# Kernel optimization log

Measured on AMD Instinct MI355X. Metric: run time of the kernel, lower is better.

## Reference

```python
import jax, jax.numpy as jnp
import numpy as np

N_NODES = 50000
N_EDGES = 1600000
N_GRAPHS = 64


def setup_inputs() -> dict:
    key = jax.random.key(0)
    ks = jax.random.split(key, 16)
    p = lambda k, shape: (jax.random.normal(k, shape, dtype=jnp.float32) * 0.05)
    x = jax.random.normal(ks[0], (N_NODES, 128), dtype=jnp.float32)
    edge_index = jax.random.randint(ks[1], (2, N_EDGES), 0, N_NODES, dtype=jnp.int32)
    edge_attr = jax.random.uniform(ks[2], (N_EDGES,), dtype=jnp.float32)
    batch = jnp.sort(jax.random.randint(ks[3], (N_NODES,), 0, N_GRAPHS, dtype=jnp.int32))
    return {
        'x': x, 'edge_index': edge_index, 'edge_attr': edge_attr, 'batch': batch,
        'W1': p(ks[4], (128, 128)), 'b1': jnp.zeros((128,), jnp.float32),
        'W2': p(ks[5], (128, 64)), 'b2': jnp.zeros((64,), jnp.float32),
        'gW1': p(ks[6], (64, 32)), 'gb1': jnp.zeros((32,), jnp.float32),
        'gW2': p(ks[7], (32, 1)), 'gb2': jnp.zeros((1,), jnp.float32),
        'fcW1': p(ks[8], (64, 128)), 'fcb1': jnp.zeros((128,), jnp.float32),
        'fcW2': p(ks[9], (128, 2)), 'fcb2': jnp.zeros((2,), jnp.float32),
    }


def gcn_conv(x, src, dst, ew, W, b):
    # PyG GCNConv with edge weights: add self-loops (weight 1), symmetric norm.
    xw = x @ W  # [N, out]
    deg = jax.ops.segment_sum(ew, dst, num_segments=N_NODES) + 1.0  # self-loop
    dinv = jnp.where(deg > 0, jax.lax.rsqrt(deg), 0.0)
    coef = dinv[src] * ew * dinv[dst]  # [E]
    agg = jax.ops.segment_sum(coef[:, None] * xw[src], dst, num_segments=N_NODES)
    agg = agg + (dinv * dinv)[:, None] * xw  # self-loop contribution
    return agg + b


def global_attention(x, batch, gW1, gb1, gW2, gb2):
    # gate_nn: Linear(64,32)->ReLU->Linear(32,1), segment-softmax over graphs
    g = (jax.nn.relu(x @ gW1 + gb1) @ gW2 + gb2)[:, 0]  # [N]
    gmax = jax.ops.segment_max(g, batch, num_segments=N_GRAPHS)
    ex = jnp.exp(g - gmax[batch])
    den = jax.ops.segment_sum(ex, batch, num_segments=N_GRAPHS)
    alpha = ex / den[batch]
    return jax.ops.segment_sum(alpha[:, None] * x, batch, num_segments=N_GRAPHS)


def reference(x, edge_index, edge_attr, batch, W1, b1, W2, b2,
              gW1, gb1, gW2, gb2, fcW1, fcb1, fcW2, fcb2):
    src, dst = edge_index[0], edge_index[1]
    h = jax.nn.relu(gcn_conv(x, src, dst, edge_attr, W1, b1))
    x1 = jax.nn.relu(gcn_conv(h, src, dst, edge_attr, W2, b2))
    x2 = global_attention(x1, batch, gW1, gb1, gW2, gb2)  # [G, 64]
    # dropout is identity in eval mode
    h2 = jax.nn.relu(x2 @ fcW1 + fcb1)
    logits = h2 @ fcW2 + fcb2
    return jax.nn.log_softmax(logits, axis=1)
```

## Files before the change

kernel.cpp:

```cpp
#include <hip/hip_runtime.h>
#include <hip/hip_bf16.h>
#include <hip/hip_fp16.h>

#define N_NODES 50000
#define N_EDGES 1600000
#define N_GRAPHS 64
#define G1BLKS 1563

__device__ __forceinline__ float coef_of(unsigned p) {
    return __half2float(__ushort_as_half((unsigned short)(p & 0xFFFFu)));
}

__global__ void mega1(const float* __restrict__ X, const float* __restrict__ W,
                      __half* __restrict__ Yh, const int* __restrict__ dst,
                      const float* __restrict__ ew,
                      unsigned long long* __restrict__ packed,
                      unsigned short* __restrict__ pos16) {
    __shared__ float Xl[32][132];
    if (blockIdx.x >= G1BLKS) {
        int e = (blockIdx.x - G1BLKS) * 256 + threadIdx.x;
        if (e < N_EDGES) {
            int d = __builtin_nontemporal_load(&dst[e]);
            float w = __builtin_nontemporal_load(&ew[e]);
            unsigned fix = (unsigned)(w * 16777216.0f);
            unsigned long long old = atomicAdd(&packed[d], 0x100000000ull | (unsigned long long)fix);
            pos16[e] = (unsigned short)(old >> 32);
        }
        return;
    }
    const int rt = threadIdx.x >> 5;
    const int ct = threadIdx.x & 31;
    const int base = blockIdx.x * 32;
    for (int i = threadIdx.x; i < 32 * 32; i += 256) {
        int rr = i >> 5, cc = (i & 31) << 2;
        int gr = base + rr;
        float4 v = (gr < N_NODES) ? *(const float4*)&X[(size_t)gr * 128 + cc]
                                  : make_float4(0.f, 0.f, 0.f, 0.f);
        Xl[rr][cc] = v.x; Xl[rr][cc + 1] = v.y; Xl[rr][cc + 2] = v.z; Xl[rr][cc + 3] = v.w;
    }
    __syncthreads();
    float acc[4][4] = {};
    for (int k = 0; k < 128; k += 4) {
        float4 a0 = *(const float4*)&Xl[rt * 4 + 0][k];
        float4 a1 = *(const float4*)&Xl[rt * 4 + 1][k];
        float4 a2 = *(const float4*)&Xl[rt * 4 + 2][k];
        float4 a3 = *(const float4*)&Xl[rt * 4 + 3][k];
        float4 w0 = *(const float4*)&W[(size_t)(k + 0) * 128 + ct * 4];
        float4 w1 = *(const float4*)&W[(size_t)(k + 1) * 128 + ct * 4];
        float4 w2 = *(const float4*)&W[(size_t)(k + 2) * 128 + ct * 4];
        float4 w3 = *(const float4*)&W[(size_t)(k + 3) * 128 + ct * 4];
        #define STEP(av, wv)  \
            acc[0][0] += av##0 * wv.x; acc[0][1] += av##0 * wv.y; acc[0][2] += av##0 * wv.z; acc[0][3] += av##0 * wv.w; \
            acc[1][0] += av##1 * wv.x; acc[1][1] += av##1 * wv.y; acc[1][2] += av##1 * wv.z; acc[1][3] += av##1 * wv.w; \
            acc[2][0] += av##2 * wv.x; acc[2][1] += av##2 * wv.y; acc[2][2] += av##2 * wv.z; acc[2][3] += av##2 * wv.w; \
            acc[3][0] += av##3 * wv.x; acc[3][1] += av##3 * wv.y; acc[3][2] += av##3 * wv.z; acc[3][3] += av##3 * wv.w;
        { float ax0=a0.x, ax1=a1.x, ax2=a2.x, ax3=a3.x; STEP(ax, w0) }
        { float ay0=a0.y, ay1=a1.y, ay2=a2.y, ay3=a3.y; STEP(ay, w1) }
        { float az0=a0.z, az1=a1.z, az2=a2.z, az3=a3.z; STEP(az, w2) }
        { float aw0=a0.w, aw1=a1.w, aw2=a2.w, aw3=a3.w; STEP(aw, w3) }
        #undef STEP
    }
    const int pc = ct >> 3;
    const int cw = (ct & 7) * 4;
    for (int i = 0; i < 4; ++i) {
        int gr = base + rt * 4 + i;
        if (gr < N_NODES) {
            ushort4 u;
            u.x = __half_as_ushort(__float2half(acc[i][0]));
            u.y = __half_as_ushort(__float2half(acc[i][1]));
            u.z = __half_as_ushort(__float2half(acc[i][2]));
            u.w = __half_as_ushort(__float2half(acc[i][3]));
            *(ushort4*)&Yh[((size_t)pc * N_NODES + gr) * 32 + cw] = u;
        }
    }
}

__global__ void block_sums_dinv(const unsigned long long* __restrict__ packed,
                                int* __restrict__ bsum, float* __restrict__ dinv) {
    __shared__ int s[256];
    int idx = blockIdx.x * 256 + threadIdx.x;
    int c = 0;
    if (idx < N_NODES) {
        unsigned long long p = packed[idx];
        c = (int)(p >> 32);
        dinv[idx] = rsqrtf((float)(unsigned)(p & 0xFFFFFFFFu) * (1.0f / 16777216.0f) + 1.0f);
    }
    s[threadIdx.x] = c;
    __syncthreads();
    for (int o = 128; o; o >>= 1) {
        if (threadIdx.x < o) s[threadIdx.x] += s[threadIdx.x + o];
        __syncthreads();
    }
    if (threadIdx.x == 0) bsum[blockIdx.x] = s[0];
}

__global__ void scan_bsums(const int* __restrict__ bsum, int* __restrict__ boff,
                           int nb, int* __restrict__ row_start_last) {
    __shared__ int s[256];
    int v = (threadIdx.x < nb) ? bsum[threadIdx.x] : 0;
    s[threadIdx.x] = v;
    __syncthreads();
    for (int o = 1; o < 256; o <<= 1) {
        int t = 0;
        if (threadIdx.x >= o) t = s[threadIdx.x - o];
        __syncthreads();
        s[threadIdx.x] += t;
        __syncthreads();
    }
    if (threadIdx.x < nb) boff[threadIdx.x] = s[threadIdx.x] - v;
    if (threadIdx.x == 0) *row_start_last = N_EDGES;
}

__global__ void scan_counts(const unsigned long long* __restrict__ packed,
                            const int* __restrict__ boff, int* __restrict__ row_start) {
    __shared__ int s[256];
    int idx = blockIdx.x * 256 + threadIdx.x;
    int v = (idx < N_NODES) ? (int)(packed[idx] >> 32) : 0;
    s[threadIdx.x] = v;
    __syncthreads();
    for (int o = 1; o < 256; o <<= 1) {
        int t = 0;
        if (threadIdx.x >= o) t = s[threadIdx.x - o];
        __syncthreads();
        s[threadIdx.x] += t;
        __syncthreads();
    }
    if (idx < N_NODES) row_start[idx] = boff[blockIdx.x] + s[threadIdx.x] - v;
}

__global__ void fill_direct(const int* __restrict__ src, const int* __restrict__ dst,
                            const float* __restrict__ ew, const unsigned short* __restrict__ pos16,
                            const int* __restrict__ row_start, const float* __restrict__ dinv,
                            unsigned* __restrict__ csr) {
    int e = blockIdx.x * 256 + threadIdx.x;
    if (e < N_EDGES) {
        int d = __builtin_nontemporal_load(&dst[e]);
        int s = __builtin_nontemporal_load(&src[e]);
        float w = __builtin_nontemporal_load(&ew[e]);
        int p = (int)__builtin_nontemporal_load(&pos16[e]);
        float coef = dinv[s] * w * dinv[d];
        csr[row_start[d] + p] = ((unsigned)s << 16) | __half_as_ushort(__float2half(coef));
    }
}

template<int NP, bool HOUT>
__global__ void agg_csr_pair(const int* __restrict__ row_start, const unsigned* __restrict__ csr,
                             const __half* __restrict__ xwh, const float* __restrict__ dinv,
                             const float* __restrict__ b, void* __restrict__ outp) {
    constexpr int OUT = NP * 32;
    const int c  = blockIdx.x % NP;
    const int nb = blockIdx.x / NP;
    const int n  = nb * 4 + (threadIdx.x >> 6);
    const int kk = threadIdx.x & 15;
    const int q  = (threadIdx.x >> 4) & 3;
    if (n >= N_NODES) return;
    const __half* __restrict__ bp = xwh + ((size_t)c * N_NODES) * 32 + 2 * kk;
    const int beg = row_start[n], end = row_start[n + 1];
    float ax = 0.f, ay = 0.f;
    int i = beg + q;
    for (; i + 12 < end; i += 16) {
        unsigned p0 = csr[i],     p1 = csr[i + 4];
        unsigned p2 = csr[i + 8], p3 = csr[i + 12];
        float2 f0 = __half22float2(*(const __half2*)(bp + (size_t)(p0 >> 16) * 32));
        float2 f1 = __half22float2(*(const __half2*)(bp + (size_t)(p1 >> 16) * 32));
        float2 f2 = __half22float2(*(const __half2*)(bp + (size_t)(p2 >> 16) * 32));
        float2 f3 = __half22float2(*(const __half2*)(bp + (size_t)(p3 >> 16) * 32));
        float e0 = coef_of(p0), e1 = coef_of(p1), e2 = coef_of(p2), e3 = coef_of(p3);
        ax += e0 * f0.x + e1 * f1.x + e2 * f2.x + e3 * f3.x;
        ay += e0 * f0.y + e1 * f1.y + e2 * f2.y + e3 * f3.y;
    }
    for (; i < end; i += 4) {
        unsigned p = csr[i];
        float2 f = __half22float2(*(const __half2*)(bp + (size_t)(p >> 16) * 32));
        float e = coef_of(p);
        ax += e * f.x; ay += e * f.y;
    }
    ax += __shfl_xor(ax, 16);  ay += __shfl_xor(ay, 16);
    ax += __shfl_xor(ax, 32);  ay += __shfl_xor(ay, 32);
    if (q == 0) {
        float2 sf = __half22float2(*(const __half2*)(bp + (size_t)n * 32));
        float dv = dinv[n];
        float dv2 = dv * dv;
        int kg = c * 32 + 2 * kk;
        float ox = fmaxf(ax + dv2 * sf.x + b[kg], 0.f);
        float oy = fmaxf(ay + dv2 * sf.y + b[kg + 1], 0.f);
        if constexpr (HOUT) {
            __half* o = (__half*)outp;
            *(__half2*)&o[(size_t)n * OUT + kg] = __floats2half2_rn(ox, oy);
        } else {
            float* o = (float*)outp;
            *(float2*)&o[(size_t)n * OUT + kg] = make_float2(ox, oy);
        }
    }
}

__global__ void gemm2_reg(const __half* __restrict__ Xh, const float* __restrict__ W,
                          __half* __restrict__ Yh, int nrows) {
    __shared__ float Xl[32][132];
    __shared__ float Wl[128][64];
    const int rt = threadIdx.x >> 5;
    const int ct = threadIdx.x & 31;
    const int base = blockIdx.x * 32;
    for (int i = threadIdx.x; i < 32 * 32; i += 256) {
        int rr = i >> 5, cc = (i & 31) << 2;
        int gr = base + rr;
        float2 fa = make_float2(0.f, 0.f), fb = fa;
        if (gr < nrows) {
            const __half2* ph = (const __half2*)&Xh[(size_t)gr * 128 + cc];
            fa = __half22float2(ph[0]);
            fb = __half22float2(ph[1]);
        }
        Xl[rr][cc] = fa.x; Xl[rr][cc + 1] = fa.y; Xl[rr][cc + 2] = fb.x; Xl[rr][cc + 3] = fb.y;
    }
    for (int i = threadIdx.x; i < 128 * 16; i += 256) {
        int kk = i >> 4, cc = (i & 15) << 2;
        *(float4*)&Wl[kk][cc] = *(const float4*)&W[(size_t)kk * 64 + cc];
    }
    float acc[4][2] = {};
    __syncthreads();
    for (int k = 0; k < 128; k += 4) {
        float4 a0 = *(const float4*)&Xl[rt * 4 + 0][k];
        float4 a1 = *(const float4*)&Xl[rt * 4 + 1][k];
        float4 a2 = *(const float4*)&Xl[rt * 4 + 2][k];
        float4 a3 = *(const float4*)&Xl[rt * 4 + 3][k];
        float2 w0 = *(const float2*)&Wl[k + 0][ct * 2];
        float2 w1 = *(const float2*)&Wl[k + 1][ct * 2];
        float2 w2 = *(const float2*)&Wl[k + 2][ct * 2];
        float2 w3 = *(const float2*)&Wl[k + 3][ct * 2];
        acc[0][0] += a0.x * w0.x; acc[0][1] += a0.x * w0.y;
        acc[1][0] += a1.x * w0.x; acc[1][1] += a1.x * w0.y;
        acc[2][0] += a2.x * w0.x; acc[2][1] += a2.x * w0.y;
        acc[3][0] += a3.x * w0.x; acc[3][1] += a3.x * w0.y;
        acc[0][0] += a0.y * w1.x; acc[0][1] += a0.y * w1.y;
        acc[1][0] += a1.y * w1.x; acc[1][1] += a1.y * w1.y;
        acc[2][0] += a2.y * w1.x; acc[2][1] += a2.y * w1.y;
        acc[3][0] += a3.y * w1.x; acc[3][1] += a3.y * w1.y;
        acc[0][0] += a0.z * w2.x; acc[0][1] += a0.z * w2.y;
        acc[1][0] += a1.z * w2.x; acc[1][1] += a1.z * w2.y;
        acc[2][0] += a2.z * w2.x; acc[2][1] += a2.z * w2.y;
        acc[3][0] += a3.z * w2.x; acc[3][1] += a3.z * w2.y;
        acc[0][0] += a0.w * w3.x; acc[0][1] += a0.w * w3.y;
        acc[1][0] += a1.w * w3.x; acc[1][1] += a1.w * w3.y;
        acc[2][0] += a2.w * w3.x; acc[2][1] += a2.w * w3.y;
        acc[3][0] += a3.w * w3.x; acc[3][1] += a3.w * w3.y;
    }
    const int col0 = ct * 2;
    const int pc   = col0 >> 5;
    const int cw   = col0 & 31;
    for (int i = 0; i < 4; ++i) {
        int gr = base + rt * 4 + i;
        if (gr < nrows) {
            __half2 hv = __floats2half2_rn(acc[i][0], acc[i][1]);
            *(__half2*)&Yh[((size_t)pc * nrows + gr) * 32 + cw] = hv;
        }
    }
}

__global__ void gate_pool(const float* __restrict__ x1, const float* __restrict__ gW1,
                          const float* __restrict__ gb1, const float* __restrict__ gW2,
                          const float* __restrict__ gb2, const int* __restrict__ batch,
                          float* __restrict__ den, float* __restrict__ pooledU) {
    __shared__ float W1l[64 * 32];
    __shared__ float W2l[32];
    __shared__ float b1l[32];
    __shared__ float el[256];
    for (int i = threadIdx.x; i < 64 * 32; i += 256) W1l[i] = gW1[i];
    if (threadIdx.x < 32) { W2l[threadIdx.x] = gW2[threadIdx.x]; b1l[threadIdx.x] = gb1[threadIdx.x]; }
    __syncthreads();
    const float gb2v = gb2[0];
    const int n0 = blockIdx.x * 256;
    const int n = n0 + threadIdx.x;
    float ev = 0.f;
    if (n < N_NODES) {
        const float* row = x1 + (size_t)n * 64;
        float t[32];
        #pragma unroll
        for (int j = 0; j < 32; ++j) t[j] = b1l[j];
        for (int k = 0; k < 64; ++k) {
            float xv = row[k];
            #pragma unroll
            for (int j = 0; j < 32; ++j) t[j] += xv * W1l[k * 32 + j];
        }
        float a = gb2v;
        #pragma unroll
        for (int j = 0; j < 32; ++j) a += fmaxf(t[j], 0.f) * W2l[j];
        ev = expf(a);
    }
    el[threadIdx.x] = ev;
    __syncthreads();
    const int f   = threadIdx.x & 63;
    const int grp = threadIdx.x >> 6;
    int start = n0 + grp * 64;
    if (start >= N_NODES) return;
    int end = min(start + 64, N_NODES);
    int cur = batch[start];
    float acc = 0.f, accd = 0.f;
    for (int m = start; m < end; ++m) {
        int bb = batch[m];
        if (bb != cur) {
            atomicAdd(&pooledU[cur * 64 + f], acc);
            if (f == 0) atomicAdd(&den[cur], accd);
            acc = 0.f; accd = 0.f; cur = bb;
        }
        float e = el[m - n0];
        acc += e * x1[(size_t)m * 64 + f];
        if (f == 0) accd += e;
    }
    atomicAdd(&pooledU[cur * 64 + f], acc);
    if (f == 0) atomicAdd(&den[cur], accd);
}

__global__ void head_kernel(const float* __restrict__ pooledU, const float* __restrict__ den,
                            const float* __restrict__ fcW1, const float* __restrict__ fcb1,
                            const float* __restrict__ fcW2, const float* __restrict__ fcb2,
                            float* __restrict__ out) {
    __shared__ float P[64];
    __shared__ float r0[2], r1[2];
    const int gi = blockIdx.x;
    if (threadIdx.x < 64) P[threadIdx.x] = pooledU[gi * 64 + threadIdx.x] / den[gi];
    __syncthreads();
    const int j = threadIdx.x;
    float a = fcb1[j];
    #pragma unroll 8
    for (int k = 0; k < 64; ++k) a += P[k] * fcW1[k * 128 + j];
    float h = fmaxf(a, 0.f);
    float p0 = h * fcW2[j * 2 + 0];
    float p1 = h * fcW2[j * 2 + 1];
    for (int o = 32; o; o >>= 1) { p0 += __shfl_xor(p0, o); p1 += __shfl_xor(p1, o); }
    if ((threadIdx.x & 63) == 0) { r0[threadIdx.x >> 6] = p0; r1[threadIdx.x >> 6] = p1; }
    __syncthreads();
    if (threadIdx.x == 0) {
        float l0 = r0[0] + r0[1] + fcb2[0];
        float l1 = r1[0] + r1[1] + fcb2[1];
        float m = fmaxf(l0, l1);
        float lse = m + logf(expf(l0 - m) + expf(l1 - m));
        out[gi * 2 + 0] = l0 - lse;
        out[gi * 2 + 1] = l1 - lse;
    }
}

extern "C" void kernel_launch(void* const* d_in, const int* in_sizes, int n_in,
                              void* d_out, int out_size, void* d_ws, size_t ws_size,
                              hipStream_t stream) {
    const float* x    = (const float*)d_in[0];
    const int*   ei   = (const int*)d_in[1];
    const float* ew   = (const float*)d_in[2];
    const int*   batch= (const int*)d_in[3];
    const float* W1   = (const float*)d_in[4];
    const float* b1   = (const float*)d_in[5];
    const float* W2   = (const float*)d_in[6];
    const float* b2   = (const float*)d_in[7];
    const float* gW1  = (const float*)d_in[8];
    const float* gb1  = (const float*)d_in[9];
    const float* gW2  = (const float*)d_in[10];
    const float* gb2  = (const float*)d_in[11];
    const float* fcW1 = (const float*)d_in[12];
    const float* fcb1 = (const float*)d_in[13];
    const float* fcW2 = (const float*)d_in[14];
    const float* fcb2 = (const float*)d_in[15];
    float* out = (float*)d_out;

    const int* src = ei;
    const int* dst = ei + N_EDGES;

    const int EB = (N_EDGES + 255) / 256;
    const int NB = (N_NODES + 255) / 256;
    const int NBLK4 = (N_NODES + 3) / 4;

    float* ws = (float*)d_ws;
    __half* xwh  = (__half*)ws;
    __half* hbuf = (__half*)(ws + 3200000);
    float*  x1   = ws + 6400000;
    size_t off = 9600000;
    unsigned* csr   = (unsigned*)(ws + off); off += 1600000;
    unsigned short* pos16 = (unsigned short*)(ws + off); off += 800000;
    int*   row_start= (int*)(ws + off);    off += 50176;
    unsigned long long* packed = (unsigned long long*)(ws + off); off += 100096;
    float* dinv     = ws + off;            off += 50176;
    int*   bsum     = (int*)(ws + off);    off += 256;
    int*   boff     = (int*)(ws + off);    off += 256;
    float* den      = ws + off;            off += 64;
    float* pooled   = ws + off;            off += 4096;

    hipMemsetAsync(packed, 0, 50048 * sizeof(unsigned long long), stream);
    hipMemsetAsync(den, 0, (64 + 4096) * sizeof(float), stream);

    mega1<<<G1BLKS + EB, 256, 0, stream>>>(x, W1, xwh, dst, ew, packed, pos16);

    block_sums_dinv<<<NB, 256, 0, stream>>>(packed, bsum, dinv);
    scan_bsums<<<1, 256, 0, stream>>>(bsum, boff, NB, row_start + N_NODES);
    scan_counts<<<NB, 256, 0, stream>>>(packed, boff, row_start);
    fill_direct<<<EB, 256, 0, stream>>>(src, dst, ew, pos16, row_start, dinv, csr);

    agg_csr_pair<4, true><<<4 * NBLK4, 256, 0, stream>>>(row_start, csr, xwh, dinv, b1, hbuf);

    gemm2_reg<<<(N_NODES + 31) / 32, 256, 0, stream>>>(hbuf, W2, xwh, N_NODES);
    agg_csr_pair<2, false><<<2 * NBLK4, 256, 0, stream>>>(row_start, csr, xwh, dinv, b2, x1);

    gate_pool<<<NB, 256, 0, stream>>>(x1, gW1, gb1, gW2, gb2, batch, den, pooled);

    head_kernel<<<N_GRAPHS, 128, 0, stream>>>(pooled, den, fcW1, fcb1, fcW2, fcb2, out);
}
```

Baseline: 341.1 us.

## Shard degree-count atomics across eight replicas to reduce contention

New measurement: 337.1 us. No clear change (-1.2%).

```diff
diff --git a/kernel.cpp b/kernel.cpp
--- a/kernel.cpp
+++ b/kernel.cpp
@@ -6,6 +6,8 @@
 #define N_EDGES 1600000
 #define N_GRAPHS 64
 #define G1BLKS 1563
+#define NSH 8
+#define SH_STRIDE 50048
 
 __device__ __forceinline__ float coef_of(unsigned p) {
     return __half2float(__ushort_as_half((unsigned short)(p & 0xFFFFu)));
@@ -14,17 +16,19 @@
 __global__ void mega1(const float* __restrict__ X, const float* __restrict__ W,
                       __half* __restrict__ Yh, const int* __restrict__ dst,
                       const float* __restrict__ ew,
-                      unsigned long long* __restrict__ packed,
+                      unsigned long long* __restrict__ packed8,
                       unsigned short* __restrict__ pos16) {
     __shared__ float Xl[32][132];
     if (blockIdx.x >= G1BLKS) {
+        const int sh = blockIdx.x & (NSH - 1);
+        unsigned long long* __restrict__ pk = packed8 + (size_t)sh * SH_STRIDE;
         int e = (blockIdx.x - G1BLKS) * 256 + threadIdx.x;
         if (e < N_EDGES) {
             int d = __builtin_nontemporal_load(&dst[e]);
             float w = __builtin_nontemporal_load(&ew[e]);
             unsigned fix = (unsigned)(w * 16777216.0f);
-            unsigned long long old = atomicAdd(&packed[d], 0x100000000ull | (unsigned long long)fix);
-            pos16[e] = (unsigned short)(old >> 32);
+            unsigned long long old = atomicAdd(&pk[d], 0x100000000ull | (unsigned long long)fix);
+            pos16[e] = (unsigned short)((sh << 12) | (unsigned)(old >> 32));
         }
         return;
     }
@@ -75,15 +79,21 @@
     }
 }
 
-__global__ void block_sums_dinv(const unsigned long long* __restrict__ packed,
+__global__ void block_sums_dinv(const unsigned long long* __restrict__ packed8,
                                 int* __restrict__ bsum, float* __restrict__ dinv) {
     __shared__ int s[256];
     int idx = blockIdx.x * 256 + threadIdx.x;
     int c = 0;
     if (idx < N_NODES) {
-        unsigned long long p = packed[idx];
-        c = (int)(p >> 32);
-        dinv[idx] = rsqrtf((float)(unsigned)(p & 0xFFFFFFFFu) * (1.0f / 16777216.0f) + 1.0f);
+        unsigned long long csum = 0, fsum = 0;
+        #pragma unroll
+        for (int sh = 0; sh < NSH; ++sh) {
+            unsigned long long p = packed8[(size_t)sh * SH_STRIDE + idx];
+            csum += p >> 32;
+            fsum += p & 0xFFFFFFFFull;
+        }
+        c = (int)csum;
+        dinv[idx] = rsqrtf((float)fsum * (1.0f / 16777216.0f) + 1.0f);
     }
     s[threadIdx.x] = c;
     __syncthreads();
@@ -111,11 +121,20 @@
     if (threadIdx.x == 0) *row_start_last = N_EDGES;
 }
 
-__global__ void scan_counts(const unsigned long long* __restrict__ packed,
-                            const int* __restrict__ boff, int* __restrict__ row_start) {
+__global__ void scan_counts(const unsigned long long* __restrict__ packed8,
+                            const int* __restrict__ boff, int* __restrict__ row_start,
+                            int* __restrict__ soff) {
     __shared__ int s[256];
     int idx = blockIdx.x * 256 + threadIdx.x;
-    int v = (idx < N_NODES) ? (int)(packed[idx] >> 32) : 0;
+    int cs[NSH];
+    int v = 0;
+    if (idx < N_NODES) {
+        #pragma unroll
+        for (int sh = 0; sh < NSH; ++sh) {
+            cs[sh] = (int)(packed8[(size_t)sh * SH_STRIDE + idx] >> 32);
+            v += cs[sh];
+        }
+    }
     s[threadIdx.x] = v;
     __syncthreads();
     for (int o = 1; o < 256; o <<= 1) {
@@ -125,21 +144,32 @@
         s[threadIdx.x] += t;
         __syncthreads();
     }
-    if (idx < N_NODES) row_start[idx] = boff[blockIdx.x] + s[threadIdx.x] - v;
+    if (idx < N_NODES) {
+        int ex = boff[blockIdx.x] + s[threadIdx.x] - v;
+        row_start[idx] = ex;
+        int run = ex;
+        #pragma unroll
+        for (int sh = 0; sh < NSH; ++sh) {
+            soff[(size_t)sh * SH_STRIDE + idx] = run;
+            run += cs[sh];
+        }
+    }
 }
 
 __global__ void fill_direct(const int* __restrict__ src, const int* __restrict__ dst,
                             const float* __restrict__ ew, const unsigned short* __restrict__ pos16,
-                            const int* __restrict__ row_start, const float* __restrict__ dinv,
+                            const int* __restrict__ soff, const float* __restrict__ dinv,
                             unsigned* __restrict__ csr) {
     int e = blockIdx.x * 256 + threadIdx.x;
     if (e < N_EDGES) {
         int d = __builtin_nontemporal_load(&dst[e]);
         int s = __builtin_nontemporal_load(&src[e]);
         float w = __builtin_nontemporal_load(&ew[e]);
-        int p = (int)__builtin_nontemporal_load(&pos16[e]);
+        unsigned p16 = (unsigned)__builtin_nontemporal_load(&pos16[e]);
+        int sh = (int)(p16 >> 12);
+        int p  = (int)(p16 & 0xFFFu);
         float coef = dinv[s] * w * dinv[d];
-        csr[row_start[d] + p] = ((unsigned)s << 16) | __half_as_ushort(__float2half(coef));
+        csr[soff[(size_t)sh * SH_STRIDE + d] + p] = ((unsigned)s << 16) | __half_as_ushort(__float2half(coef));
     }
 }
 
@@ -375,22 +405,23 @@
     unsigned* csr   = (unsigned*)(ws + off); off += 1600000;
     unsigned short* pos16 = (unsigned short*)(ws + off); off += 800000;
     int*   row_start= (int*)(ws + off);    off += 50176;
-    unsigned long long* packed = (unsigned long long*)(ws + off); off += 100096;
+    unsigned long long* packed8 = (unsigned long long*)(ws + off); off += 2 * NSH * SH_STRIDE;
+    int*   soff     = (int*)(ws + off);    off += NSH * SH_STRIDE;
     float* dinv     = ws + off;            off += 50176;
     int*   bsum     = (int*)(ws + off);    off += 256;
     int*   boff     = (int*)(ws + off);    off += 256;
     float* den      = ws + off;            off += 64;
     float* pooled   = ws + off;            off += 4096;
 
-    hipMemsetAsync(packed, 0, 50048 * sizeof(unsigned long long), stream);
+    hipMemsetAsync(packed8, 0, (size_t)NSH * SH_STRIDE * sizeof(unsigned long long), stream);
     hipMemsetAsync(den, 0, (64 + 4096) * sizeof(float), stream);
 
-    mega1<<<G1BLKS + EB, 256, 0, stream>>>(x, W1, xwh, dst, ew, packed, pos16);
-
-    block_sums_dinv<<<NB, 256, 0, stream>>>(packed, bsum, dinv);
+    mega1<<<G1BLKS + EB, 256, 0, stream>>>(x, W1, xwh, dst, ew, packed8, pos16);
+
+    block_sums_dinv<<<NB, 256, 0, stream>>>(packed8, bsum, dinv);
     scan_bsums<<<1, 256, 0, stream>>>(bsum, boff, NB, row_start + N_NODES);
-    scan_counts<<<NB, 256, 0, stream>>>(packed, boff, row_start);
-    fill_direct<<<EB, 256, 0, stream>>>(src, dst, ew, pos16, row_start, dinv, csr);
+    scan_counts<<<NB, 256, 0, stream>>>(packed8, boff, row_start, soff);
+    fill_direct<<<EB, 256, 0, stream>>>(src, dst, ew, pos16, soff, dinv, csr);
 
     agg_csr_pair<4, true><<<4 * NBLK4, 256, 0, stream>>>(row_start, csr, xwh, dinv, b1, hbuf);
 
```
